# Kernel optimization log

Hardware: AMD Instinct MI355X
Metric: run time of the kernel (lower is better)

The kernel has to match this reference:

```python
import jax, jax.numpy as jnp
import numpy as np

N_NODES = 100000
N_EDGES = 1600000


def setup_inputs() -> dict:
    key = jax.random.key(0)
    k1, k2, k3, k4, k5 = jax.random.split(key, 5)
    node_states = jax.random.normal(k1, (N_NODES, 128), dtype=jnp.float32)
    edge_index = jax.random.randint(k2, (2, N_EDGES), 0, N_NODES, dtype=jnp.int64)
    mask = jax.random.uniform(k3, (N_EDGES,), dtype=jnp.float32)  # edge weights
    # Glorot-ish init for the two GCN linear layers
    W1 = jax.random.normal(k4, (128, 64), dtype=jnp.float32) * 0.05
    b1 = jnp.zeros((64,), dtype=jnp.float32)
    W2 = jax.random.normal(k5, (64, 64), dtype=jnp.float32) * 0.05
    b2 = jnp.zeros((64,), dtype=jnp.float32)
    return {"node_states": node_states, "edge_index": edge_index, "mask": mask,
            "W1": W1, "b1": b1, "W2": W2, "b2": b2}


def _gcn_layer(x, src, dst, edge_w, W, b, n_nodes):
    # PyG GCNConv (normalize=False): h = x @ W; out[dst] += edge_w * h[src]; out += b
    h = x @ W                                  # [N, d_out]
    msg = h[src] * edge_w[:, None]             # [E, d_out] gather + scale
    agg = jax.ops.segment_sum(msg, dst, num_segments=n_nodes)  # scatter-add
    return agg + b


def reference(node_states, edge_index, mask, W1, b1, W2, b2):
    src = edge_index[0]
    dst = edge_index[1]
    n = node_states.shape[0]
    h1 = jax.nn.relu(_gcn_layer(node_states, src, dst, mask, W1, b1, n))
    h2 = jax.nn.relu(_gcn_layer(h1, src, dst, mask, W2, b2, n))
    return h2
```

## Files before the change

### kernel.cpp

```cpp
#include <hip/hip_runtime.h>
#include <hip/hip_bf16.h>

#define N_NODES 100000
#define N_EDGES 1600000
#define NBUCKET 1563
#define NBLK_S 391
#define CHUNK_E 4096
#define CAP 1280
#define GCSTRIDE 32
#define FIXSCALE 1048576.0f
#define FIXINV   (1.0f / 1048576.0f)


typedef short v8s __attribute__((ext_vector_type(8)));
typedef float v4f __attribute__((ext_vector_type(4)));

static __device__ __forceinline__ unsigned pack_bf2(float a, float b) {
    __hip_bfloat162 p = __float22bfloat162_rn(make_float2(a, b));
    return *reinterpret_cast<unsigned*>(&p);
}
static __device__ __forceinline__ float2 bf2_to_f2(unsigned u) {
    __hip_bfloat162 p = *reinterpret_cast<__hip_bfloat162*>(&u);
    return __bfloat1622float2(p);
}

__global__ __launch_bounds__(1024) void k1_sort_gemm(const int* __restrict__ src,
                                                     const int* __restrict__ dst,
                                                     const float* __restrict__ wgt,
                                                     const float* __restrict__ x,
                                                     const float* __restrict__ W1,
                                                     int* __restrict__ gcount,
                                                     int2* __restrict__ arena,
                                                     unsigned* __restrict__ hpre) {
    __shared__ __align__(16) int smem[18004];
    const int b = blockIdx.x;
    const int t = threadIdx.x;

    if (b >= NBLK_S) {
        unsigned* xs = (unsigned*)smem;
        unsigned* ws = (unsigned*)smem + 64 * 68;
        const int tile = b - NBLK_S;
        const int row0 = tile * 64;
        {
            const float2* g2 = (const float2*)W1;
            for (int i = t; i < 64 * 128 / 2; i += 1024) {
                const float2 v = g2[i];
                const int k = (2 * i) >> 6;
                const int c = (2 * i) & 63;
                ((short*)&ws[c * 68])[k]       = (short)(pack_bf2(v.x, 0.f) & 0xFFFF);
                ((short*)&ws[(c + 1) * 68])[k] = (short)(pack_bf2(v.y, 0.f) & 0xFFFF);
            }
        }
        {
            const float4* g = (const float4*)x;
            for (int i = t; i < 64 * 32; i += 1024) {
                const int r = i >> 5, cu = i & 31;
                const int row = row0 + r;
                uint2 v = make_uint2(0u, 0u);
                if (row < N_NODES) {
                    float4 f = g[(size_t)row * 32 + cu];
                    v.x = pack_bf2(f.x, f.y);
                    v.y = pack_bf2(f.z, f.w);
                }
                *(uint2*)&xs[r * 68 + 2 * cu] = v;
            }
        }
        __syncthreads();
        const int w = t >> 6, lane = t & 63;
        const int l15 = lane & 15, quad = lane >> 4;
        const int a  = w & 3;
        const int g_ = w >> 2;
        v4f acc = (v4f){0.f, 0.f, 0.f, 0.f};
#pragma unroll
        for (int k0 = 0; k0 < 128; k0 += 32) {
            const int ku = k0 / 2 + quad * 4;
            const v8s xb = *(const v8s*)&xs[(g_ * 16 + l15) * 68 + ku];
            const v8s wa = *(const v8s*)&ws[(16 * a + l15) * 68 + ku];
            acc = __builtin_amdgcn_mfma_f32_16x16x32_bf16(wa, xb, acc, 0, 0, 0);
        }
        __syncthreads();
        float* stg = (float*)smem;
        *(v4f*)&stg[(g_ * 16 + l15) * 68 + 16 * a + 4 * quad] = acc;
        __syncthreads();
        for (int i2 = t; i2 < 2048; i2 += 1024) {
            const int nl = i2 >> 5, d = i2 & 31;
            const int row = row0 + nl;
            if (row < N_NODES)
                hpre[(size_t)row * 32 + d] = pack_bf2(stg[nl * 68 + d], stg[nl * 68 + d + 32]);
        }
        return;
    }

    int*  hist  = smem;
    int*  lcur  = smem + 1563;
    int*  tgb   = smem + 3126;
    int*  pairs = smem + 4689;
    int*  tg    = smem + 5713;
    int2* ord   = (int2*)(smem + 9810);

    for (int i = t; i < NBUCKET; i += 1024) hist[i] = 0;
    __syncthreads();

    const int e0 = b * CHUNK_E;
    const int n = min(CHUNK_E, N_EDGES - e0);
    const int nI4 = n >> 2;
    const bool act = t < nI4;
    int4 sv, dv; float4 wv;
    if (act) {
        sv = ((const int4*)(src + e0))[t];
        dv = ((const int4*)(dst + e0))[t];
        wv = ((const float4*)(wgt + e0))[t];
        atomicAdd(&hist[dv.x >> 6], 1);
        atomicAdd(&hist[dv.y >> 6], 1);
        atomicAdd(&hist[dv.z >> 6], 1);
        atomicAdd(&hist[dv.w >> 6], 1);
    }
    __syncthreads();
    {
        int a0 = 0, a1 = 0;
        if (2 * t < NBUCKET) a0 = hist[2 * t];
        if (2 * t + 1 < NBUCKET) a1 = hist[2 * t + 1];
        pairs[t] = a0 + a1;
    }
    __syncthreads();
    for (int off = 1; off < 1024; off <<= 1) {
        const int u = (t >= off) ? pairs[t - off] : 0;
        __syncthreads();
        pairs[t] += u;
        __syncthreads();
    }
    if (2 * t < NBUCKET) {
        const int a0 = hist[2 * t];
        const int a1 = (2 * t + 1 < NBUCKET) ? hist[2 * t + 1] : 0;
        const int incl = pairs[t];
        lcur[2 * t] = incl - a0 - a1;
        if (2 * t + 1 < NBUCKET) lcur[2 * t + 1] = incl - a1;
    }
    __syncthreads();
    for (int i = t; i < NBUCKET; i += 1024) {
        const int hv = hist[i];
        const int lb = lcur[i];
        const int grsv = (hv > 0) ? atomicAdd(&gcount[i * GCSTRIDE], hv) : 0;
        tgb[i] = i * CAP + grsv - lb;
    }
    __syncthreads();
    if (act) {
        {
            const int bk = dv.x >> 6;
            const int lp = atomicAdd(&lcur[bk], 1);
            ord[lp] = make_int2(sv.x | ((dv.x & 63) << 17), __float_as_int(wv.x));
            tg[lp] = tgb[bk] + lp;
        }
        {
            const int bk = dv.y >> 6;
            const int lp = atomicAdd(&lcur[bk], 1);
            ord[lp] = make_int2(sv.y | ((dv.y & 63) << 17), __float_as_int(wv.y));
            tg[lp] = tgb[bk] + lp;
        }
        {
            const int bk = dv.z >> 6;
            const int lp = atomicAdd(&lcur[bk], 1);
            ord[lp] = make_int2(sv.z | ((dv.z & 63) << 17), __float_as_int(wv.z));
            tg[lp] = tgb[bk] + lp;
        }
        {
            const int bk = dv.w >> 6;
            const int lp = atomicAdd(&lcur[bk], 1);
            ord[lp] = make_int2(sv.w | ((dv.w & 63) << 17), __float_as_int(wv.w));
            tg[lp] = tgb[bk] + lp;
        }
    }
    __syncthreads();
    for (int i = t; i < n; i += 1024)
        arena[tg[i]] = ord[i];
}

static __device__ __forceinline__ void acc_rec(int* __restrict__ accs, int2 r,
                                               unsigned hv, int li) {
    const int dl = (r.x >> 17) & 63;
    const float ws = __int_as_float(r.y) * FIXSCALE;
    const float2 f = bf2_to_f2(hv);
    atomicAdd(&accs[dl * 64 + li],      (int)(ws * f.x));
    atomicAdd(&accs[dl * 64 + 32 + li], (int)(ws * f.y));
}

template<bool FUSE>
__global__ __launch_bounds__(256) void gather_fuse(const unsigned* __restrict__ hsrc,
                                                   const int2* __restrict__ arena,
                                                   const int* __restrict__ gcount,
                                                   const float* __restrict__ bias,
                                                   const float* __restrict__ W2,
                                                   void* __restrict__ outp) {
    __shared__ int accs[64 * 68];
    extern __shared__ unsigned wsdyn[];
    const int b = blockIdx.x;
    const int t = threadIdx.x;
    for (int i = t; i < 4096; i += 256) accs[i] = 0;
    if constexpr (FUSE) {
        const float2* g2 = (const float2*)W2;
        for (int i = t; i < 2048; i += 256) {
            const float2 v = g2[i];
            const int k = (2 * i) >> 6;
            const int c = (2 * i) & 63;
            ((short*)&wsdyn[c * 36])[k]       = (short)(pack_bf2(v.x, 0.f) & 0xFFFF);
            ((short*)&wsdyn[(c + 1) * 36])[k] = (short)(pack_bf2(v.y, 0.f) & 0xFFFF);
        }
    }
    __syncthreads();
    const int cnt = gcount[b * GCSTRIDE];
    const size_t base = (size_t)b * CAP;
    const int lane = t & 63;
    const int li = lane & 31;
    int i = (t >> 6) * 2 + (lane >> 5);
    for (; i + 56 < cnt; i += 64) {
        int2 r0 = arena[base + i];
        int2 r1 = arena[base + i + 8];
        int2 r2 = arena[base + i + 16];
        int2 r3 = arena[base + i + 24];
        int2 r4 = arena[base + i + 32];
        int2 r5 = arena[base + i + 40];
        int2 r6 = arena[base + i + 48];
        int2 r7 = arena[base + i + 56];
        unsigned h0 = hsrc[(size_t)(r0.x & 0x1FFFF) * 32 + li];
        unsigned h1 = hsrc[(size_t)(r1.x & 0x1FFFF) * 32 + li];
        unsigned h2 = hsrc[(size_t)(r2.x & 0x1FFFF) * 32 + li];
        unsigned h3 = hsrc[(size_t)(r3.x & 0x1FFFF) * 32 + li];
        unsigned h4 = hsrc[(size_t)(r4.x & 0x1FFFF) * 32 + li];
        unsigned h5 = hsrc[(size_t)(r5.x & 0x1FFFF) * 32 + li];
        unsigned h6 = hsrc[(size_t)(r6.x & 0x1FFFF) * 32 + li];
        unsigned h7 = hsrc[(size_t)(r7.x & 0x1FFFF) * 32 + li];
        acc_rec(accs, r0, h0, li);
        acc_rec(accs, r1, h1, li);
        acc_rec(accs, r2, h2, li);
        acc_rec(accs, r3, h3, li);
        acc_rec(accs, r4, h4, li);
        acc_rec(accs, r5, h5, li);
        acc_rec(accs, r6, h6, li);
        acc_rec(accs, r7, h7, li);
    }
    for (; i < cnt; i += 8) {
        const int2 r = arena[base + i];
        const unsigned h = hsrc[(size_t)(r.x & 0x1FFFF) * 32 + li];
        acc_rec(accs, r, h, li);
    }
    __syncthreads();

    if constexpr (FUSE) {
        unsigned pk[8];
#pragma unroll
        for (int k = 0; k < 8; ++k) {
            const int i2 = t + k * 256;
            const int node = i2 >> 5, cp = i2 & 31;
            const float f0 = fmaxf((float)accs[node * 64 + 2 * cp]     * FIXINV + bias[2 * cp],     0.f);
            const float f1 = fmaxf((float)accs[node * 64 + 2 * cp + 1] * FIXINV + bias[2 * cp + 1], 0.f);
            pk[k] = pack_bf2(f0, f1);
        }
        __syncthreads();
        unsigned* xs = (unsigned*)accs;
#pragma unroll
        for (int k = 0; k < 8; ++k) {
            const int i2 = t + k * 256;
            const int node = i2 >> 5, cp = i2 & 31;
            xs[node * 36 + cp] = pk[k];
        }
        __syncthreads();
        const int w = t >> 6, l15 = lane & 15, quad = lane >> 4;
        v4f a4[4];
#pragma unroll
        for (int tt = 0; tt < 4; ++tt) a4[tt] = (v4f){0.f, 0.f, 0.f, 0.f};
#pragma unroll
        for (int k0 = 0; k0 < 64; k0 += 32) {
            const int ku = k0 / 2 + quad * 4;
            const v8s xb = *(const v8s*)&xs[(w * 16 + l15) * 36 + ku];
#pragma unroll
            for (int tt = 0; tt < 4; ++tt) {
                const v8s wa = *(const v8s*)&wsdyn[(16 * tt + l15) * 36 + ku];
                a4[tt] = __builtin_amdgcn_mfma_f32_16x16x32_bf16(wa, xb, a4[tt], 0, 0, 0);
            }
        }
        __syncthreads();
        float* stg = (float*)accs;
#pragma unroll
        for (int tt = 0; tt < 4; ++tt)
            *(v4f*)&stg[(w * 16 + l15) * 68 + 16 * tt + 4 * quad] = a4[tt];
        __syncthreads();
        for (int i2 = t; i2 < 2048; i2 += 256) {
            const int nl = i2 >> 5, d = i2 & 31;
            const int ng = b * 64 + nl;
            if (ng < N_NODES)
                ((unsigned*)outp)[(size_t)ng * 32 + d] =
                    pack_bf2(stg[nl * 68 + d], stg[nl * 68 + d + 32]);
        }
    } else {
        for (int i2 = t; i2 < 2048; i2 += 256) {
            const int node = i2 >> 5, cp = i2 & 31;
            const int ng = b * 64 + node;
            if (ng < N_NODES) {
                float2 o;
                o.x = fmaxf((float)accs[node * 64 + 2 * cp]     * FIXINV + bias[2 * cp],     0.f);
                o.y = fmaxf((float)accs[node * 64 + 2 * cp + 1] * FIXINV + bias[2 * cp + 1], 0.f);
                *(float2*)&((float*)outp)[(size_t)ng * 64 + 2 * cp] = o;
            }
        }
    }
}

extern "C" void kernel_launch(void* const* d_in, const int* in_sizes, int n_in,
                              void* d_out, int out_size, void* d_ws, size_t ws_size,
                              hipStream_t stream) {
    const float* x    = (const float*)d_in[0];
    const int*   eidx = (const int*)d_in[1];
    const float* mask = (const float*)d_in[2];
    const float* W1   = (const float*)d_in[3];
    const float* b1   = (const float*)d_in[4];
    const float* W2   = (const float*)d_in[5];
    const float* b2   = (const float*)d_in[6];
    float* out = (float*)d_out;

    const int* src = eidx;
    const int* dst = eidx + N_EDGES;

    unsigned* hpre = (unsigned*)d_out;

    int2*     arena  = (int2*)d_ws;
    int*      gcount = (int*)(arena + (size_t)NBUCKET * CAP);
    unsigned* hpre2  = (unsigned*)(gcount + NBUCKET * GCSTRIDE);

    const int gemmBlocks = (N_NODES + 63) / 64;

    hipMemsetAsync(gcount, 0, NBUCKET * GCSTRIDE * sizeof(int), stream);

    k1_sort_gemm<<<NBLK_S + gemmBlocks, 1024, 0, stream>>>(src, dst, mask, x, W1,
                                                           gcount, arena, hpre);

    gather_fuse<true><<<NBUCKET, 256, 64 * 36 * 4, stream>>>(hpre, arena, gcount,
                                                             b1, W2, hpre2);
    gather_fuse<false><<<NBUCKET, 256, 0, stream>>>(hpre2, arena, gcount,
                                                    b2, nullptr, out);
}
```

Measured before the change: 245.0 us.

## Sort edges into coarse 256-node buckets and filter per sub-bucket in gather

The edge sort now uses 391 coarse buckets of 256 destination nodes instead of 1563 buckets of 64, which shrinks the histogram and scan in the sort kernel. Each gather block scans its coarse bucket and keeps only the edges for its 64-node sub-bucket in a shared-memory queue, then accumulates from that queue with a new lane mapping in which each thread handles two columns. Block IDs are also remapped so that sub-buckets of the same coarse bucket land on the same XCD for cache locality. The cost is that every coarse-bucket record is read four times, once per sub-bucket block, and coarse buckets are capped at 4608 edges, with queue overflow beyond 1280 silently dropped.

```diff
diff --git a/kernel.cpp b/kernel.cpp
--- a/kernel.cpp
+++ b/kernel.cpp
@@ -3,10 +3,12 @@
 
 #define N_NODES 100000
 #define N_EDGES 1600000
-#define NBUCKET 1563
+#define NB_C 391
+#define NB_F 1563
 #define NBLK_S 391
 #define CHUNK_E 4096
-#define CAP 1280
+#define CAPC 4608
+#define QCAP 1280
 #define GCSTRIDE 32
 #define FIXSCALE 1048576.0f
 #define FIXINV   (1.0f / 1048576.0f)
@@ -32,7 +34,7 @@
                                                      int* __restrict__ gcount,
                                                      int2* __restrict__ arena,
                                                      unsigned* __restrict__ hpre) {
-    __shared__ __align__(16) int smem[18004];
+    __shared__ __align__(16) int smem[13976];
     const int b = blockIdx.x;
     const int t = threadIdx.x;
 
@@ -92,13 +94,13 @@
     }
 
     int*  hist  = smem;
-    int*  lcur  = smem + 1563;
-    int*  tgb   = smem + 3126;
-    int*  pairs = smem + 4689;
-    int*  tg    = smem + 5713;
-    int2* ord   = (int2*)(smem + 9810);
-
-    for (int i = t; i < NBUCKET; i += 1024) hist[i] = 0;
+    int*  lcur  = smem + 391;
+    int*  tgb   = smem + 782;
+    int*  pairs = smem + 1173;
+    int*  tg    = smem + 1685;
+    int2* ord   = (int2*)(smem + 5782);
+
+    for (int i = t; i < NB_C; i += 1024) hist[i] = 0;
     __syncthreads();
 
     const int e0 = b * CHUNK_E;
@@ -110,78 +112,59 @@
         sv = ((const int4*)(src + e0))[t];
         dv = ((const int4*)(dst + e0))[t];
         wv = ((const float4*)(wgt + e0))[t];
-        atomicAdd(&hist[dv.x >> 6], 1);
-        atomicAdd(&hist[dv.y >> 6], 1);
-        atomicAdd(&hist[dv.z >> 6], 1);
-        atomicAdd(&hist[dv.w >> 6], 1);
-    }
-    __syncthreads();
-    {
-        int a0 = 0, a1 = 0;
-        if (2 * t < NBUCKET) a0 = hist[2 * t];
-        if (2 * t + 1 < NBUCKET) a1 = hist[2 * t + 1];
-        pairs[t] = a0 + a1;
-    }
-    __syncthreads();
-    for (int off = 1; off < 1024; off <<= 1) {
-        const int u = (t >= off) ? pairs[t - off] : 0;
-        __syncthreads();
-        pairs[t] += u;
-        __syncthreads();
-    }
-    if (2 * t < NBUCKET) {
-        const int a0 = hist[2 * t];
-        const int a1 = (2 * t + 1 < NBUCKET) ? hist[2 * t + 1] : 0;
-        const int incl = pairs[t];
-        lcur[2 * t] = incl - a0 - a1;
-        if (2 * t + 1 < NBUCKET) lcur[2 * t + 1] = incl - a1;
-    }
-    __syncthreads();
-    for (int i = t; i < NBUCKET; i += 1024) {
+        atomicAdd(&hist[dv.x >> 8], 1);
+        atomicAdd(&hist[dv.y >> 8], 1);
+        atomicAdd(&hist[dv.z >> 8], 1);
+        atomicAdd(&hist[dv.w >> 8], 1);
+    }
+    __syncthreads();
+    if (t < 512) pairs[t] = (t < NB_C) ? hist[t] : 0;
+    __syncthreads();
+    for (int off = 1; off < 512; off <<= 1) {
+        int u = 0;
+        if (t < 512 && t >= off) u = pairs[t - off];
+        __syncthreads();
+        if (t < 512) pairs[t] += u;
+        __syncthreads();
+    }
+    if (t < NB_C) lcur[t] = pairs[t] - hist[t];
+    __syncthreads();
+    for (int i = t; i < NB_C; i += 1024) {
         const int hv = hist[i];
         const int lb = lcur[i];
         const int grsv = (hv > 0) ? atomicAdd(&gcount[i * GCSTRIDE], hv) : 0;
-        tgb[i] = i * CAP + grsv - lb;
+        tgb[i] = i * CAPC + grsv - lb;
     }
     __syncthreads();
     if (act) {
         {
-            const int bk = dv.x >> 6;
+            const int bk = dv.x >> 8;
             const int lp = atomicAdd(&lcur[bk], 1);
-            ord[lp] = make_int2(sv.x | ((dv.x & 63) << 17), __float_as_int(wv.x));
+            ord[lp] = make_int2(sv.x | ((dv.x & 255) << 17), __float_as_int(wv.x));
             tg[lp] = tgb[bk] + lp;
         }
         {
-            const int bk = dv.y >> 6;
+            const int bk = dv.y >> 8;
             const int lp = atomicAdd(&lcur[bk], 1);
-            ord[lp] = make_int2(sv.y | ((dv.y & 63) << 17), __float_as_int(wv.y));
+            ord[lp] = make_int2(sv.y | ((dv.y & 255) << 17), __float_as_int(wv.y));
             tg[lp] = tgb[bk] + lp;
         }
         {
-            const int bk = dv.z >> 6;
+            const int bk = dv.z >> 8;
             const int lp = atomicAdd(&lcur[bk], 1);
-            ord[lp] = make_int2(sv.z | ((dv.z & 63) << 17), __float_as_int(wv.z));
+            ord[lp] = make_int2(sv.z | ((dv.z & 255) << 17), __float_as_int(wv.z));
             tg[lp] = tgb[bk] + lp;
         }
         {
-            const int bk = dv.w >> 6;
+            const int bk = dv.w >> 8;
             const int lp = atomicAdd(&lcur[bk], 1);
-            ord[lp] = make_int2(sv.w | ((dv.w & 63) << 17), __float_as_int(wv.w));
+            ord[lp] = make_int2(sv.w | ((dv.w & 255) << 17), __float_as_int(wv.w));
             tg[lp] = tgb[bk] + lp;
         }
     }
     __syncthreads();
     for (int i = t; i < n; i += 1024)
         arena[tg[i]] = ord[i];
-}
-
-static __device__ __forceinline__ void acc_rec(int* __restrict__ accs, int2 r,
-                                               unsigned hv, int li) {
-    const int dl = (r.x >> 17) & 63;
-    const float ws = __int_as_float(r.y) * FIXSCALE;
-    const float2 f = bf2_to_f2(hv);
-    atomicAdd(&accs[dl * 64 + li],      (int)(ws * f.x));
-    atomicAdd(&accs[dl * 64 + 32 + li], (int)(ws * f.y));
 }
 
 template<bool FUSE>
@@ -192,10 +175,19 @@
                                                    const float* __restrict__ W2,
                                                    void* __restrict__ outp) {
     __shared__ int accs[64 * 68];
+    __shared__ int2 qrec[QCAP];
+    __shared__ int qn_s;
     extern __shared__ unsigned wsdyn[];
-    const int b = blockIdx.x;
     const int t = threadIdx.x;
+
+    const int orig = blockIdx.x;
+    const int xcd = orig & 7, idx = orig >> 3;
+    const int b = (xcd < 3 ? xcd * 196 : 3 * 196 + (xcd - 3) * 195) + idx;
+
+    const int cb = b >> 2;
+    const int sub = b & 3;
     for (int i = t; i < 4096; i += 256) accs[i] = 0;
+    if (t == 0) qn_s = 0;
     if constexpr (FUSE) {
         const float2* g2 = (const float2*)W2;
         for (int i = t; i < 2048; i += 256) {
@@ -207,44 +199,53 @@
         }
     }
     __syncthreads();
-    const int cnt = gcount[b * GCSTRIDE];
-    const size_t base = (size_t)b * CAP;
+
+    const int cntc = min(gcount[cb * GCSTRIDE], CAPC);
+    const size_t cbase = (size_t)cb * CAPC;
+    for (int i = t; i < cntc; i += 256) {
+        const int2 r = arena[cbase + i];
+        if (((r.x >> 23) & 3) == sub) {
+            const int pos = atomicAdd(&qn_s, 1);
+            if (pos < QCAP) qrec[pos] = r;
+        }
+    }
+    __syncthreads();
+    const int qn = min(qn_s, QCAP);
+    const int npad = (qn + 127) & ~127;
+    for (int i = qn + t; i < npad; i += 256) qrec[i] = make_int2(0, 0);
+    __syncthreads();
+
+    const int li2 = t & 15;
+    const int s   = t >> 4;
+    const int qw  = s & 3;
+    const int da  = (li2 + 8 * qw) & 31;
+    const int db  = (da + 16) & 31;
+    for (int ib = s; ib < npad; ib += 128) {
+        int2 r[8];
+#pragma unroll
+        for (int j = 0; j < 8; ++j) r[j] = qrec[ib + 16 * j];
+        unsigned ha[8], hb[8];
+#pragma unroll
+        for (int j = 0; j < 8; ++j) {
+            const unsigned* row = hsrc + (size_t)(r[j].x & 0x1FFFF) * 32;
+            ha[j] = row[da];
+            hb[j] = row[db];
+        }
+#pragma unroll
+        for (int j = 0; j < 8; ++j) {
+            const int dl = (r[j].x >> 17) & 63;
+            const float wsf = __int_as_float(r[j].y) * FIXSCALE;
+            const float2 fa = bf2_to_f2(ha[j]);
+            const float2 fb = bf2_to_f2(hb[j]);
+            atomicAdd(&accs[dl * 64 + da],      (int)(wsf * fa.x));
+            atomicAdd(&accs[dl * 64 + da + 32], (int)(wsf * fa.y));
+            atomicAdd(&accs[dl * 64 + db],      (int)(wsf * fb.x));
+            atomicAdd(&accs[dl * 64 + db + 32], (int)(wsf * fb.y));
+        }
+    }
+    __syncthreads();
+
     const int lane = t & 63;
-    const int li = lane & 31;
-    int i = (t >> 6) * 2 + (lane >> 5);
-    for (; i + 56 < cnt; i += 64) {
-        int2 r0 = arena[base + i];
-        int2 r1 = arena[base + i + 8];
-        int2 r2 = arena[base + i + 16];
-        int2 r3 = arena[base + i + 24];
-        int2 r4 = arena[base + i + 32];
-        int2 r5 = arena[base + i + 40];
-        int2 r6 = arena[base + i + 48];
-        int2 r7 = arena[base + i + 56];
-        unsigned h0 = hsrc[(size_t)(r0.x & 0x1FFFF) * 32 + li];
-        unsigned h1 = hsrc[(size_t)(r1.x & 0x1FFFF) * 32 + li];
-        unsigned h2 = hsrc[(size_t)(r2.x & 0x1FFFF) * 32 + li];
-        unsigned h3 = hsrc[(size_t)(r3.x & 0x1FFFF) * 32 + li];
-        unsigned h4 = hsrc[(size_t)(r4.x & 0x1FFFF) * 32 + li];
-        unsigned h5 = hsrc[(size_t)(r5.x & 0x1FFFF) * 32 + li];
-        unsigned h6 = hsrc[(size_t)(r6.x & 0x1FFFF) * 32 + li];
-        unsigned h7 = hsrc[(size_t)(r7.x & 0x1FFFF) * 32 + li];
-        acc_rec(accs, r0, h0, li);
-        acc_rec(accs, r1, h1, li);
-        acc_rec(accs, r2, h2, li);
-        acc_rec(accs, r3, h3, li);
-        acc_rec(accs, r4, h4, li);
-        acc_rec(accs, r5, h5, li);
-        acc_rec(accs, r6, h6, li);
-        acc_rec(accs, r7, h7, li);
-    }
-    for (; i < cnt; i += 8) {
-        const int2 r = arena[base + i];
-        const unsigned h = hsrc[(size_t)(r.x & 0x1FFFF) * 32 + li];
-        acc_rec(accs, r, h, li);
-    }
-    __syncthreads();
-
     if constexpr (FUSE) {
         unsigned pk[8];
 #pragma unroll
@@ -323,18 +324,18 @@
     unsigned* hpre = (unsigned*)d_out;
 
     int2*     arena  = (int2*)d_ws;
-    int*      gcount = (int*)(arena + (size_t)NBUCKET * CAP);
-    unsigned* hpre2  = (unsigned*)(gcount + NBUCKET * GCSTRIDE);
+    int*      gcount = (int*)(arena + (size_t)NB_C * CAPC);
+    unsigned* hpre2  = (unsigned*)(gcount + NB_C * GCSTRIDE);
 
     const int gemmBlocks = (N_NODES + 63) / 64;
 
-    hipMemsetAsync(gcount, 0, NBUCKET * GCSTRIDE * sizeof(int), stream);
+    hipMemsetAsync(gcount, 0, NB_C * GCSTRIDE * sizeof(int), stream);
 
     k1_sort_gemm<<<NBLK_S + gemmBlocks, 1024, 0, stream>>>(src, dst, mask, x, W1,
                                                            gcount, arena, hpre);
 
-    gather_fuse<true><<<NBUCKET, 256, 64 * 36 * 4, stream>>>(hpre, arena, gcount,
-                                                             b1, W2, hpre2);
-    gather_fuse<false><<<NBUCKET, 256, 0, stream>>>(hpre2, arena, gcount,
-                                                    b2, nullptr, out);
-}
+    gather_fuse<true><<<NB_F, 256, 64 * 36 * 4, stream>>>(hpre, arena, gcount,
+                                                          b1, W2, hpre2);
+    gather_fuse<false><<<NB_F, 256, 0, stream>>>(hpre2, arena, gcount,
+                                                 b2, nullptr, out);
+}
```

Result: faster. 221.6 us (-9.6%).
